# Optimization experiments

Hardware: AMD Instinct MI355X
Metric: run time of the kernel (lower is better)

The kernel has to match this reference:

```python
import jax
import jax.numpy as jnp
from jax import lax
import numpy as np

B, T, IN, H, K = 8, 4096, 512, 512, 2


def setup_inputs() -> dict:
    key = jax.random.key(0)
    k = jax.random.split(key, 5)
    scale_w0 = 1.0 / np.sqrt(IN * K)
    scale_w1 = 1.0 / np.sqrt(H * K)
    return {
        "x": jax.random.normal(k[0], (B, T, IN), jnp.float32),
        "w0": jax.random.normal(k[1], (3 * H, IN, K), jnp.float32) * scale_w0,
        "b0": jax.random.normal(k[2], (3 * H,), jnp.float32) * scale_w0,
        "w1": jax.random.normal(k[3], (3 * H, H, K), jnp.float32) * scale_w1,
        "b1": jax.random.normal(k[4], (3 * H,), jnp.float32) * scale_w1,
    }


def _qrnn_layer(x, w, b):
    # x: [B, T, C]; w: [3H, C, K]; causal conv (left pad K-1), matching
    # torch padding=K-1 then slicing off the last K-1 timesteps.
    xc = jnp.transpose(x, (0, 2, 1))  # [B, C, T]
    conv = lax.conv_general_dilated(
        xc, w, window_strides=(1,), padding=[(K - 1, 0)],
        dimension_numbers=("NCH", "OIH", "NCH"))
    conv = conv + b[None, :, None]
    conv = jnp.transpose(conv, (0, 2, 1))  # [B, T, 3H]
    z, f, o = jnp.split(conv, 3, axis=-1)
    z = jnp.tanh(z)
    f = jax.nn.sigmoid(f)
    o = jax.nn.sigmoid(o)

    def step(h, zfo):
        zt, ft, ot = zfo
        h = ft * h + (1.0 - ft) * zt  # fo-pool recurrence
        return h, ot * h

    h0 = jnp.zeros((x.shape[0], z.shape[-1]), x.dtype)
    hT, outs = lax.scan(
        step, h0,
        (jnp.swapaxes(z, 0, 1), jnp.swapaxes(f, 0, 1), jnp.swapaxes(o, 0, 1)))
    return jnp.swapaxes(outs, 0, 1), hT  # [B, T, H], [B, H]


def reference(x, w0, b0, w1, b1):
    out, h0 = _qrnn_layer(x, w0, b0)
    out, h1 = _qrnn_layer(out, w1, b1)
    return out, h0, h1
```

## Files before the change

### kernel.cpp

```cpp
#include <hip/hip_runtime.h>
#include <cstdint>

#define B_ 8
#define T_ 4096
#define TP1 4097
#define IN_ 512
#define H_ 512
#define N3H 1536
#define KD 1024
#define CHUNKS 64
#define CLEN 64

typedef __attribute__((ext_vector_type(4))) float floatx4;
typedef __attribute__((ext_vector_type(4))) float f4;
typedef __attribute__((ext_vector_type(8))) short short8;
typedef __attribute__((ext_vector_type(4))) unsigned short us4;
typedef __attribute__((ext_vector_type(4))) _Float16 h4;

__device__ __forceinline__ unsigned short f2bf(float v){
  unsigned int u = __float_as_uint(v);
  unsigned int r = (u + 0x7fffu + ((u >> 16) & 1u)) >> 16;
  return (unsigned short)r;
}
__device__ __forceinline__ float sigm(float x){
  return __builtin_amdgcn_rcpf(1.f + __expf(-x));
}
__device__ __forceinline__ float tanhf_(float x){ return 2.f*sigm(2.f*x) - 1.f; }

#define GLLS(src, dst) __builtin_amdgcn_global_load_lds( \
    (const __attribute__((address_space(1))) void*)(src), \
    (__attribute__((address_space(3))) void*)(dst), 16, 0, 0)

__global__ void cast_pad_kernel(const float* __restrict__ x, unsigned short* __restrict__ xpad){
  int64_t i = (int64_t)blockIdx.x*256 + threadIdx.x;
  const int64_t total = (int64_t)B_*TP1*(IN_/4);
  if (i >= total) return;
  int cg = (int)(i & 127);
  int64_t r = i >> 7;
  int t = (int)(r % TP1);
  int b = (int)(r / TP1);
  us4 o;
  if (t == 0){ o = (us4){0,0,0,0}; }
  else {
    f4 v = *(const f4*)(x + ((int64_t)b*T_ + (t-1))*IN_ + cg*4);
    #pragma unroll
    for (int u=0;u<4;++u) o[u] = f2bf(v[u]);
  }
  *(us4*)(xpad + r*IN_ + cg*4) = o;
}

__global__ void wt_kernel(const float* __restrict__ wA, unsigned short* __restrict__ wtA,
                          const float* __restrict__ wB, unsigned short* __restrict__ wtB){
  int i = blockIdx.x*256 + threadIdx.x;
  if (i >= N3H*512) return;
  const float* w = blockIdx.y ? wB : wA;
  unsigned short* wt = blockIdx.y ? wtB : wtA;
  int ci = i & 511;
  int o = i >> 9;
  const float* wp = w + (int64_t)o*KD + ci*2;
  wt[(int64_t)o*KD + ci]       = f2bf(wp[0]);
  wt[(int64_t)o*KD + 512 + ci] = f2bf(wp[1]);
}

__global__ __launch_bounds__(256) void gemm_kernel(
    const unsigned short* __restrict__ A, const unsigned short* __restrict__ W,
    const float* __restrict__ bias, _Float16* __restrict__ C){
  __shared__ unsigned short As[128*32];
  __shared__ unsigned short Bs[128*32];
  const int tid = threadIdx.x;
  const int lane = tid & 63;
  const int wave = tid >> 6;
  const int bid = blockIdx.x;
  const int xcd = bid & 7;
  const int kb  = bid >> 3;
  const int colt = kb % 12;
  const int rowt = (kb / 12) * 8 + xcd;
  const int m0 = rowt * 128;
  const int n0 = colt * 128;
  const int bb = m0 / T_;
  const int act = n0 >> 9;
  const unsigned short* aSrc = A + (int64_t)(m0 + bb + (tid>>2))*IN_ + (tid&3)*8;
  const unsigned short* bSrc = W + (int64_t)(n0 + (tid>>2))*KD + (tid&3)*8;
  unsigned short* aDst = As + tid*8;
  unsigned short* bDst = Bs + tid*8;
  const int wm = wave & 1;
  const int wn = wave >> 1;
  const int l16 = lane & 15;
  const int quad = lane >> 4;
  floatx4 acc[4][4];
  #pragma unroll
  for (int i=0;i<4;i++)
    #pragma unroll
    for (int j=0;j<4;j++) acc[i][j] = (floatx4){0.f,0.f,0.f,0.f};
  const unsigned short* aLds = As + (wm*64 + l16)*32 + quad*8;
  const unsigned short* bLds = Bs + (wn*64 + l16)*32 + quad*8;

  for (int kk = 0; kk < KD; kk += 32){
    __syncthreads();
    GLLS(aSrc + kk,           aDst);
    GLLS(aSrc + 64*IN_ + kk,  aDst + 2048);
    GLLS(bSrc + kk,           bDst);
    GLLS(bSrc + 64*KD + kk,   bDst + 2048);
    __syncthreads();
    short8 af[4], bfr[4];
    #pragma unroll
    for (int i=0;i<4;i++) af[i] = *(const short8*)(aLds + i*16*32);
    #pragma unroll
    for (int j=0;j<4;j++) bfr[j] = *(const short8*)(bLds + j*16*32);
    #pragma unroll
    for (int i=0;i<4;i++)
      #pragma unroll
      for (int j=0;j<4;j++)
        acc[i][j] = __builtin_amdgcn_mfma_f32_16x16x32_bf16(af[i], bfr[j], acc[i][j], 0, 0, 0);
  }
  float bv[4];
  #pragma unroll
  for (int j=0;j<4;j++) bv[j] = bias[n0 + wn*64 + j*16 + l16];
  #pragma unroll
  for (int i=0;i<4;i++){
    int row = m0 + wm*64 + i*16 + quad*4;
    #pragma unroll
    for (int j=0;j<4;j++){
      int col = n0 + wn*64 + j*16 + l16;
      _Float16* cp = C + (int64_t)row*N3H + col;
      #pragma unroll
      for (int r=0;r<4;r++){
        float v = acc[i][j][r] + bv[j];
        v = (act == 0) ? tanhf_(v) : sigm(v);
        cp[(int64_t)r*N3H] = (_Float16)v;
      }
    }
  }
}

__global__ void scan_phase1(const _Float16* __restrict__ conv,
                            float* __restrict__ carA, float* __restrict__ carB){
  int q = blockIdx.x*256 + threadIdx.x;
  int chg = q & 127;
  int bq = (q >> 7) & 7;
  int c  = q >> 10;
  int ch = chg*4;
  f4 Aa = {1.f,1.f,1.f,1.f}, Bb = {0.f,0.f,0.f,0.f};
  const _Float16* p = conv + ((int64_t)bq*T_ + c*CLEN)*N3H + ch;
  for (int g=0; g<CLEN/8; ++g){
    h4 zb[8], fb[8];
    #pragma unroll
    for (int u=0;u<8;++u){
      zb[u] = *(const h4*)(p + (int64_t)u*N3H);
      fb[u] = *(const h4*)(p + (int64_t)u*N3H + 512);
    }
    #pragma unroll
    for (int u=0;u<8;++u){
      #pragma unroll
      for (int v=0;v<4;++v){
        float fv = (float)fb[u][v];
        float zv = (float)zb[u][v];
        Aa[v] *= fv;
        Bb[v] = fv*Bb[v] + (1.f-fv)*zv;
      }
    }
    p += (int64_t)8*N3H;
  }
  *(f4*)(carA + (int64_t)q*4) = Aa;
  *(f4*)(carB + (int64_t)q*4) = Bb;
}

__global__ void scan_phase2(const float* __restrict__ carA, const float* __restrict__ carB,
                            float* __restrict__ hstart, float* __restrict__ hT){
  int q = blockIdx.x*256 + threadIdx.x;
  float h = 0.f;
  for (int c=0;c<CHUNKS;++c){
    int64_t idx = (int64_t)c*4096 + q;
    hstart[idx] = h;
    h = carA[idx]*h + carB[idx];
  }
  hT[q] = h;
}

template<int LAYER>
__global__ void scan_phase3(const _Float16* __restrict__ conv,
                            const float* __restrict__ hstart, unsigned short* __restrict__ xpad,
                            float* __restrict__ outf){
  int q = blockIdx.x*256 + threadIdx.x;
  int chg = q & 127;
  int bq = (q >> 7) & 7;
  int c  = q >> 10;
  int ch = chg*4;
  f4 h;
  #pragma unroll
  for (int v=0;v<4;++v) h[v] = hstart[(int64_t)c*4096 + bq*512 + ch + v];
  const _Float16* p = conv + ((int64_t)bq*T_ + c*CLEN)*N3H + ch;
  int t = c*CLEN;
  for (int g=0; g<CLEN/8; ++g){
    h4 zb[8], fb[8], ob[8];
    #pragma unroll
    for (int u=0;u<8;++u){
      zb[u] = *(const h4*)(p + (int64_t)u*N3H);
      fb[u] = *(const h4*)(p + (int64_t)u*N3H + 512);
      ob[u] = *(const h4*)(p + (int64_t)u*N3H + 1024);
    }
    #pragma unroll
    for (int u=0;u<8;++u){
      if (LAYER == 0){
        us4 ov4;
        #pragma unroll
        for (int v=0;v<4;++v){
          float fv = (float)fb[u][v];
          h[v] = fv*h[v] + (1.f-fv)*(float)zb[u][v];
          ov4[v] = f2bf((float)ob[u][v]*h[v]);
        }
        *(us4*)(xpad + ((int64_t)bq*TP1 + t+u + 1)*IN_ + ch) = ov4;
      } else {
        f4 of4;
        #pragma unroll
        for (int v=0;v<4;++v){
          float fv = (float)fb[u][v];
          h[v] = fv*h[v] + (1.f-fv)*(float)zb[u][v];
          of4[v] = (float)ob[u][v]*h[v];
        }
        *(f4*)(outf + ((int64_t)bq*T_ + t+u)*H_ + ch) = of4;
      }
    }
    t += 8; p += (int64_t)8*N3H;
  }
}

extern "C" void kernel_launch(void* const* d_in, const int* in_sizes, int n_in,
                              void* d_out, int out_size, void* d_ws, size_t ws_size,
                              hipStream_t stream){
  const float* x  = (const float*)d_in[0];
  const float* w0 = (const float*)d_in[1];
  const float* b0 = (const float*)d_in[2];
  const float* w1 = (const float*)d_in[3];
  const float* b1 = (const float*)d_in[4];
  float* out = (float*)d_out;

  char* ws = (char*)d_ws;
  size_t off = 0;
  auto alloc = [&](size_t bytes)->char*{
    char* p = ws + off; off = (off + bytes + 255) & ~(size_t)255; return p; };
  unsigned short* xpad = (unsigned short*)alloc((size_t)B_*TP1*IN_*2);
  unsigned short* Wt0  = (unsigned short*)alloc((size_t)N3H*KD*2);
  unsigned short* Wt1  = (unsigned short*)alloc((size_t)N3H*KD*2);
  _Float16* conv = (_Float16*)alloc((size_t)B_*T_*N3H*2);
  float* carA = (float*)alloc((size_t)CHUNKS*4096*4);
  float* carB = (float*)alloc((size_t)CHUNKS*4096*4);
  float* hst  = (float*)alloc((size_t)CHUNKS*4096*4);
  if (off > ws_size) return;

  float* out_main = out;
  float* h0 = out + (int64_t)B_*T_*H_;
  float* h1 = h0 + B_*H_;

  const int64_t padN = (int64_t)B_*TP1*(IN_/4);
  cast_pad_kernel<<<(int)((padN + 255)/256), 256, 0, stream>>>(x, xpad);
  dim3 wgrid((N3H*512 + 255)/256, 2);
  wt_kernel<<<wgrid, 256, 0, stream>>>(w0, Wt0, w1, Wt1);

  const int ggrid = (N3H/128) * ((B_*T_)/128);
  const int sgrid = (CHUNKS*8*128) / 256;
  gemm_kernel<<<ggrid, 256, 0, stream>>>(xpad, Wt0, b0, conv);
  scan_phase1<<<sgrid, 256, 0, stream>>>(conv, carA, carB);
  scan_phase2<<<16, 256, 0, stream>>>(carA, carB, hst, h0);
  scan_phase3<0><<<sgrid, 256, 0, stream>>>(conv, hst, xpad, nullptr);

  gemm_kernel<<<ggrid, 256, 0, stream>>>(xpad, Wt1, b1, conv);
  scan_phase1<<<sgrid, 256, 0, stream>>>(conv, carA, carB);
  scan_phase2<<<16, 256, 0, stream>>>(carA, carB, hst, h1);
  scan_phase3<1><<<sgrid, 256, 0, stream>>>(conv, hst, nullptr, out_main);
}
```

Measured before the change: 453.9 us.

## Rewrite conv GEMM with 256x256 tiles, double-buffered LDS pipeline and swizzle

Restructures the bf16 MFMA GEMM to 256x256 output tiles with 512 threads and a 64-wide K step. LDS is double-buffered, and global-to-LDS loads for the next tiles are interleaved between quarter-tile MFMA phases using fine-grained barriers, vmcnt waits and s_setprio. An XOR swizzle on the LDS layout is meant to avoid bank conflicts. The aim is to hide load latency and raise arithmetic intensity per block. The cost is 128KB of LDS, heavier register use and more complex synchronisation.

```diff
diff --git a/kernel.cpp b/kernel.cpp
--- a/kernel.cpp
+++ b/kernel.cpp
@@ -10,6 +10,7 @@
 #define KD 1024
 #define CHUNKS 64
 #define CLEN 64
+#define NT 16
 
 typedef __attribute__((ext_vector_type(4))) float floatx4;
 typedef __attribute__((ext_vector_type(4))) float f4;
@@ -62,70 +63,131 @@
   wt[(int64_t)o*KD + 512 + ci] = f2bf(wp[1]);
 }
 
-__global__ __launch_bounds__(256) void gemm_kernel(
+#define MFMA(a,b,c) __builtin_amdgcn_mfma_f32_16x16x32_bf16(a,b,c,0,0,0)
+#define BAR() __builtin_amdgcn_s_barrier()
+
+#define ST_A(tt, h) do { \
+    const unsigned short* _s = aSrc + (h)*128*IN_ + (tt)*64; \
+    unsigned short* _d = smem + ((tt)&1)*16384 + (h)*8192 + dstBase; \
+    GLLS(_s, _d); GLLS(_s + 64*IN_, _d + 4096); } while(0)
+#define ST_B(tt, h) do { \
+    const unsigned short* _s = bSrc + (h)*128*KD + (tt)*64; \
+    unsigned short* _d = smem + 32768 + ((tt)&1)*16384 + (h)*8192 + dstBase; \
+    GLLS(_s, _d); GLLS(_s + 64*KD, _d + 4096); } while(0)
+
+#define LDA(d,h,i,s) (*(const short8*)(smem + (d)*16384 + (h)*8192 + aRd + (i)*1024 + (s)))
+#define LDB(d,h,i,s) (*(const short8*)(smem + (d)*16384 + (h)*8192 + bRd + (i)*1024 + (s)))
+
+#define TILE(tc, SA1, SB1, SA0, SB0, VMN) do { \
+  const int d_ = (tc) & 1; \
+   \
+  _Pragma("unroll") for (int i=0;i<4;++i){ aF[i][0]=LDA(d_,0,i,sw0); aF[i][1]=LDA(d_,0,i,sw1); } \
+  _Pragma("unroll") for (int j=0;j<2;++j){ bF0[j][0]=LDB(d_,0,j,sw0); bF0[j][1]=LDB(d_,0,j,sw1); } \
+  if (SA1) ST_A((tc)+1, 1); \
+  BAR(); \
+  __builtin_amdgcn_s_setprio(1); \
+  _Pragma("unroll") for (int i=0;i<4;++i) _Pragma("unroll") for (int j=0;j<2;++j){ \
+    acc[i][j]=MFMA(aF[i][0],bF0[j][0],acc[i][j]); acc[i][j]=MFMA(aF[i][1],bF0[j][1],acc[i][j]); } \
+  __builtin_amdgcn_s_setprio(0); \
+  BAR(); \
+   \
+  _Pragma("unroll") for (int j=0;j<2;++j){ bF1[j][0]=LDB(d_,1,j,sw0); bF1[j][1]=LDB(d_,1,j,sw1); } \
+  if (SB1) ST_B((tc)+1, 1); \
+  BAR(); \
+  __builtin_amdgcn_s_setprio(1); \
+  _Pragma("unroll") for (int i=0;i<4;++i) _Pragma("unroll") for (int j=0;j<2;++j){ \
+    acc[i][2+j]=MFMA(aF[i][0],bF1[j][0],acc[i][2+j]); acc[i][2+j]=MFMA(aF[i][1],bF1[j][1],acc[i][2+j]); } \
+  __builtin_amdgcn_s_setprio(0); \
+  BAR(); \
+   \
+  _Pragma("unroll") for (int i=0;i<4;++i){ aF[i][0]=LDA(d_,1,i,sw0); aF[i][1]=LDA(d_,1,i,sw1); } \
+  if (SA0) ST_A((tc)+2, 0); \
+  BAR(); \
+  __builtin_amdgcn_s_setprio(1); \
+  _Pragma("unroll") for (int i=0;i<4;++i) _Pragma("unroll") for (int j=0;j<2;++j){ \
+    acc[4+i][j]=MFMA(aF[i][0],bF0[j][0],acc[4+i][j]); acc[4+i][j]=MFMA(aF[i][1],bF0[j][1],acc[4+i][j]); } \
+  __builtin_amdgcn_s_setprio(0); \
+  BAR(); \
+   \
+  if (SB0) ST_B((tc)+2, 0); \
+  BAR(); \
+  __builtin_amdgcn_s_setprio(1); \
+  _Pragma("unroll") for (int i=0;i<4;++i) _Pragma("unroll") for (int j=0;j<2;++j){ \
+    acc[4+i][2+j]=MFMA(aF[i][0],bF1[j][0],acc[4+i][2+j]); acc[4+i][2+j]=MFMA(aF[i][1],bF1[j][1],acc[4+i][2+j]); } \
+  __builtin_amdgcn_s_setprio(0); \
+  if ((VMN)==4) asm volatile("s_waitcnt vmcnt(4)" ::: "memory"); \
+  else if ((VMN)==0) asm volatile("s_waitcnt vmcnt(0)" ::: "memory"); \
+  BAR(); \
+} while(0)
+
+__global__ __launch_bounds__(512, 2) void gemm_kernel(
     const unsigned short* __restrict__ A, const unsigned short* __restrict__ W,
     const float* __restrict__ bias, _Float16* __restrict__ C){
-  __shared__ unsigned short As[128*32];
-  __shared__ unsigned short Bs[128*32];
-  const int tid = threadIdx.x;
+  __shared__ unsigned short smem[65536];
+  const int tid  = threadIdx.x;
   const int lane = tid & 63;
   const int wave = tid >> 6;
+  const int l16  = lane & 15;
+  const int quad = lane >> 4;
+  const int wm = wave >> 2;
+  const int wn = wave & 3;
+  const int lrow = lane >> 3;
+  const int lcol = lane & 7;
+
   const int bid = blockIdx.x;
-  const int xcd = bid & 7;
-  const int kb  = bid >> 3;
-  const int colt = kb % 12;
-  const int rowt = (kb / 12) * 8 + xcd;
-  const int m0 = rowt * 128;
-  const int n0 = colt * 128;
+  const int wg = (bid & 7) * 96 + (bid >> 3);
+  const int mt = wg / 6;
+  const int nt = wg % 6;
+  const int m0 = mt * 256;
+  const int n0 = nt * 256;
   const int bb = m0 / T_;
   const int act = n0 >> 9;
-  const unsigned short* aSrc = A + (int64_t)(m0 + bb + (tid>>2))*IN_ + (tid&3)*8;
-  const unsigned short* bSrc = W + (int64_t)(n0 + (tid>>2))*KD + (tid&3)*8;
-  unsigned short* aDst = As + tid*8;
-  unsigned short* bDst = Bs + tid*8;
-  const int wm = wave & 1;
-  const int wn = wave >> 1;
-  const int l16 = lane & 15;
-  const int quad = lane >> 4;
-  floatx4 acc[4][4];
+
+  const unsigned short* aSrc = A + (int64_t)(m0 + bb + wave*8 + lrow)*IN_ + (lcol ^ lrow)*8;
+  const unsigned short* bSrc = W + (int64_t)(n0 + wave*8 + lrow)*KD + (lcol ^ lrow)*8;
+  const int dstBase = (wave*8 + lrow)*64 + lcol*8;
+
+  const int sw0 = ( quad      ^ (l16 & 7)) * 8;
+  const int sw1 = ((4 ^ quad) ^ (l16 & 7)) * 8;
+  const int aRd = (wm*64 + l16)*64;
+  const int bRd = 32768 + (wn*32 + l16)*64;
+
+  floatx4 acc[8][4];
   #pragma unroll
-  for (int i=0;i<4;i++)
+  for (int i=0;i<8;i++)
     #pragma unroll
     for (int j=0;j<4;j++) acc[i][j] = (floatx4){0.f,0.f,0.f,0.f};
-  const unsigned short* aLds = As + (wm*64 + l16)*32 + quad*8;
-  const unsigned short* bLds = Bs + (wn*64 + l16)*32 + quad*8;
-
-  for (int kk = 0; kk < KD; kk += 32){
-    __syncthreads();
-    GLLS(aSrc + kk,           aDst);
-    GLLS(aSrc + 64*IN_ + kk,  aDst + 2048);
-    GLLS(bSrc + kk,           bDst);
-    GLLS(bSrc + 64*KD + kk,   bDst + 2048);
-    __syncthreads();
-    short8 af[4], bfr[4];
-    #pragma unroll
-    for (int i=0;i<4;i++) af[i] = *(const short8*)(aLds + i*16*32);
-    #pragma unroll
-    for (int j=0;j<4;j++) bfr[j] = *(const short8*)(bLds + j*16*32);
-    #pragma unroll
-    for (int i=0;i<4;i++)
-      #pragma unroll
-      for (int j=0;j<4;j++)
-        acc[i][j] = __builtin_amdgcn_mfma_f32_16x16x32_bf16(af[i], bfr[j], acc[i][j], 0, 0, 0);
-  }
+  short8 aF[4][2], bF0[2][2], bF1[2][2];
+
+  ST_A(0,0); ST_B(0,0); ST_A(0,1); ST_B(0,1); ST_A(1,0); ST_B(1,0);
+  asm volatile("s_waitcnt vmcnt(4)" ::: "memory");
+  BAR();
+
+  #pragma unroll 2
+  for (int t = 0; t < NT-2; ++t){
+    TILE(t, 1, 1, 1, 1, 4);
+  }
+  TILE(NT-2, 1, 1, 0, 0, 0);
+  TILE(NT-1, 0, 0, 0, 0, -1);
+
   float bv[4];
   #pragma unroll
-  for (int j=0;j<4;j++) bv[j] = bias[n0 + wn*64 + j*16 + l16];
+  for (int n=0;n<4;++n){
+    const int cb = ((n&2)?128:0) + wn*32 + (n&1)*16;
+    bv[n] = bias[n0 + cb + l16];
+  }
   #pragma unroll
-  for (int i=0;i<4;i++){
-    int row = m0 + wm*64 + i*16 + quad*4;
-    #pragma unroll
-    for (int j=0;j<4;j++){
-      int col = n0 + wn*64 + j*16 + l16;
+  for (int m=0;m<8;++m){
+    const int rb = ((m&4)?128:0) + wm*64 + (m&3)*16;
+    const int row = m0 + rb + quad*4;
+    #pragma unroll
+    for (int n=0;n<4;++n){
+      const int cb = ((n&2)?128:0) + wn*32 + (n&1)*16;
+      const int col = n0 + cb + l16;
       _Float16* cp = C + (int64_t)row*N3H + col;
       #pragma unroll
-      for (int r=0;r<4;r++){
-        float v = acc[i][j][r] + bv[j];
+      for (int r=0;r<4;++r){
+        float v = acc[m][n][r] + bv[n];
         v = (act == 0) ? tanhf_(v) : sigm(v);
         cp[(int64_t)r*N3H] = (_Float16)v;
       }
@@ -257,14 +319,14 @@
   dim3 wgrid((N3H*512 + 255)/256, 2);
   wt_kernel<<<wgrid, 256, 0, stream>>>(w0, Wt0, w1, Wt1);
 
-  const int ggrid = (N3H/128) * ((B_*T_)/128);
+  const int ggrid = ((B_*T_)/256) * (N3H/256);
   const int sgrid = (CHUNKS*8*128) / 256;
-  gemm_kernel<<<ggrid, 256, 0, stream>>>(xpad, Wt0, b0, conv);
+  gemm_kernel<<<ggrid, 512, 0, stream>>>(xpad, Wt0, b0, conv);
   scan_phase1<<<sgrid, 256, 0, stream>>>(conv, carA, carB);
   scan_phase2<<<16, 256, 0, stream>>>(carA, carB, hst, h0);
   scan_phase3<0><<<sgrid, 256, 0, stream>>>(conv, hst, xpad, nullptr);
 
-  gemm_kernel<<<ggrid, 256, 0, stream>>>(xpad, Wt1, b1, conv);
+  gemm_kernel<<<ggrid, 512, 0, stream>>>(xpad, Wt1, b1, conv);
   scan_phase1<<<sgrid, 256, 0, stream>>>(conv, carA, carB);
   scan_phase2<<<16, 256, 0, stream>>>(carA, carB, hst, h1);
   scan_phase3<1><<<sgrid, 256, 0, stream>>>(conv, hst, nullptr, out_main);
```

Result: faster. 414.6 us (-8.7%).
